# Performance work log

Measured on AMD Instinct MI355X. Metric: run time of the kernel, lower is better.

Reference implementation:

```python
import jax, jax.numpy as jnp
import numpy as np
from jax.scipy.special import logsumexp

B, T, N = 512, 1024, 64


def setup_inputs() -> dict:
    key = jax.random.key(0)
    k1, k2, k3, k4, k5, k6 = jax.random.split(key, 6)
    emit = jax.random.normal(k1, (B, T, N), dtype=jnp.float32)
    target = jax.random.randint(k2, (B, T), 0, N)
    # valid monotone mask: each sequence has length in [T//2, T], length >= 1
    lengths = jax.random.randint(k3, (B,), T // 2, T + 1)
    mask = jnp.arange(T)[None, :] < lengths[:, None]  # [B, T] bool
    trans = 0.1 * jax.random.normal(k4, (N, N), dtype=jnp.float32)
    strans = 0.1 * jax.random.normal(k5, (N,), dtype=jnp.float32)
    etrans = 0.1 * jax.random.normal(k6, (N,), dtype=jnp.float32)
    return {"emit": emit, "target": target, "mask": mask,
            "trans": trans, "strans": strans, "etrans": etrans}


def _get_logZ(emit_t, mask_t, trans, strans, etrans):
    # emit_t: [T, B, N], mask_t: [T, B]
    alpha0 = strans[None, :] + emit_t[0]  # [B, N]

    def step(alpha, inp):
        e_i, m_i = inp  # [B, N], [B]
        # scores[b, j] = logsumexp_i(alpha[b, i] + trans[i, j] + e_i[b, j])
        scores = logsumexp(alpha[:, :, None] + trans[None, :, :], axis=1) + e_i
        alpha = jnp.where(m_i[:, None], scores, alpha)
        return alpha, None

    alpha, _ = jax.lax.scan(step, alpha0, (emit_t[1:], mask_t[1:]))
    logZ = logsumexp(alpha + etrans[None, :], axis=1).sum()
    return logZ / B


def _get_score(emit_t, target_t, mask_t, trans, strans, etrans):
    # emit_t: [T, B, N], target_t/mask_t: [T, B]
    emit_scores = jnp.take_along_axis(emit_t, target_t[:, :, None], axis=2)[:, :, 0]  # [T, B]
    trans_scores = trans[target_t[:-1], target_t[1:]]  # [T-1, B]
    scores = emit_scores.at[1:].add(trans_scores)
    score = jnp.where(mask_t, scores, 0.0).sum()
    ends = mask_t.sum(axis=0) - 1  # [B]
    score = score + strans[target_t[0]].sum()
    last_tags = target_t[ends, jnp.arange(target_t.shape[1])]
    score = score + etrans[last_tags].sum()
    return score / B


def reference(emit, target, mask, trans, strans, etrans):
    # batch_first=True -> move to time-major [T, B, ...]
    emit_t = jnp.swapaxes(emit, 0, 1)
    target_t = target.T
    mask_t = mask.T
    logZ = _get_logZ(emit_t, mask_t, trans, strans, etrans)
    score = _get_score(emit_t, target_t, mask_t, trans, strans, etrans)
    return logZ - score
```

## Files before the change

kernel.cpp:

```cpp
#include <hip/hip_runtime.h>

#define Bn 512
#define Tn 1024
#define Nn 64
#define Kseg 8
#define BURN 16

typedef _Float16 h2 __attribute__((ext_vector_type(2)));
typedef _Float16 h8 __attribute__((ext_vector_type(8)));

#if __has_builtin(__builtin_amdgcn_fdot2)
__device__ __forceinline__ float fdot2f(h2 a, h2 b, float c) {
    return __builtin_amdgcn_fdot2(a, b, c, false);
}
#else
__device__ __forceinline__ float fdot2f(h2 a, h2 b, float c) {
    return fmaf((float)a[0], (float)b[0], fmaf((float)a[1], (float)b[1], c));
}
#endif

__device__ __forceinline__ float wave_sum(float v) {
#pragma unroll
    for (int off = 32; off >= 1; off >>= 1) v += __shfl_xor(v, off, 64);
    return v;
}

__global__ __launch_bounds__(64) void crf_seg(
    const float* __restrict__ emit,
    const int*   __restrict__ target,
    const int*   __restrict__ mask,
    const float* __restrict__ trans,
    const float* __restrict__ strans,
    const float* __restrict__ etrans,
    float*       __restrict__ out)
{
    __shared__ __align__(16) _Float16 pbuf[Nn];

    const int lane = threadIdx.x;
    const int b    = blockIdx.x & (Bn - 1);
    const int s    = blockIdx.x >> 9;

    h2 E2[32];
#pragma unroll
    for (int m = 0; m < 32; ++m) {
        float x0 = trans[(2 * m) * Nn + lane];
        float x1 = trans[(2 * m + 1) * Nn + lane];
        h2 e; e[0] = (_Float16)__expf(x0); e[1] = (_Float16)__expf(x1);
        E2[m] = e;
    }

    const int* mrow = mask + (size_t)b * Tn;
    int lsum = 0;
#pragma unroll
    for (int k = 0; k < Tn / Nn; ++k) lsum += mrow[k * Nn + lane];
#pragma unroll
    for (int off = 32; off >= 1; off >>= 1) lsum += __shfl_xor(lsum, off, 64);
    const int len = lsum;

    const int a_s = (s * len) >> 3;
    const int a_e = ((s + 1) * len) >> 3;
    const int tb   = s ? (a_s - BURN) : 1;
    const int tend = a_e - 1;
    const int rec_t = s ? a_s : -1;

    const size_t ebase = (size_t)b * Tn * Nn;

    float uu = s ? 1.0f : __expf(strans[lane]);
    int   S  = 0;
    float L0 = 0.0f;

    float wC[8], eN[8];
#pragma unroll
    for (int q = 0; q < 8; ++q) wC[q] = emit[ebase + (size_t)(tb - 1 + q) * Nn + lane];
#pragma unroll
    for (int q = 0; q < 8; ++q) eN[q] = emit[ebase + (size_t)(tb + 7 + q) * Nn + lane];
#pragma unroll
    for (int q = 0; q < 8; ++q) wC[q] = __expf(wC[q]);

    auto step = [&](float w) {
        int bits = __builtin_amdgcn_readfirstlane(__float_as_int(uu));
        int mk   = 127 - ((bits >> 23) & 0xff);
        S += mk;
        float p = ldexpf(uu, mk) * w;
        pbuf[lane] = (_Float16)p;

        const h8* pb8 = (const h8*)pbuf;
        float a0 = 0.f, a1 = 0.f, a2 = 0.f, a3 = 0.f;
        float a4 = 0.f, a5 = 0.f, a6 = 0.f, a7 = 0.f;
#pragma unroll
        for (int r = 0; r < 8; r += 2) {
            h8 v0 = pb8[r], v1 = pb8[r + 1];
            a0 = fdot2f(__builtin_shufflevector(v0, v0, 0, 1), E2[4 * r + 0], a0);
            a1 = fdot2f(__builtin_shufflevector(v0, v0, 2, 3), E2[4 * r + 1], a1);
            a2 = fdot2f(__builtin_shufflevector(v0, v0, 4, 5), E2[4 * r + 2], a2);
            a3 = fdot2f(__builtin_shufflevector(v0, v0, 6, 7), E2[4 * r + 3], a3);
            a4 = fdot2f(__builtin_shufflevector(v1, v1, 0, 1), E2[4 * r + 4], a4);
            a5 = fdot2f(__builtin_shufflevector(v1, v1, 2, 3), E2[4 * r + 5], a5);
            a6 = fdot2f(__builtin_shufflevector(v1, v1, 4, 5), E2[4 * r + 6], a6);
            a7 = fdot2f(__builtin_shufflevector(v1, v1, 6, 7), E2[4 * r + 7], a7);
        }
        uu = ((a0 + a1) + (a2 + a3)) + ((a4 + a5) + (a6 + a7));
    };

    int t0 = tb;
    while (t0 + 8 <= tend + 1) {
#pragma unroll
        for (int q = 0; q < 8; ++q) step(wC[q]);
#pragma unroll
        for (int q = 0; q < 8; ++q) wC[q] = __expf(eN[q]);
#pragma unroll
        for (int q = 0; q < 8; ++q) {
            int idx = t0 + 15 + q; if (idx > tend - 1) idx = tend - 1;
            eN[q] = emit[ebase + (size_t)idx * Nn + lane];
        }
        t0 += 8;
        if (t0 == rec_t) {
            L0 = __logf(wave_sum(uu));
            S = 0;
        }
    }
#pragma unroll
    for (int q = 0; q < 8; ++q)
        if (t0 + q <= tend) step(wC[q]);

    float lend;
    if (s == Kseg - 1) {
        float eL = emit[ebase + (size_t)(len - 1) * Nn + lane];
        lend = __logf(wave_sum(uu * __expf(eL + etrans[lane])));
    } else {
        lend = __logf(wave_sum(uu));
    }
    float contrib = lend - (float)S * 0.6931471805599453f - L0;

    const int* trow = target + (size_t)b * Tn;
    const int t_sc = s ? a_s : 0;
    float sc = 0.0f;
#pragma unroll
    for (int k = 0; k < 3; ++k) {
        int t = t_sc + k * Nn + lane;
        if (t < a_e) {
            int g = trow[t];
            sc += emit[ebase + (size_t)t * Nn + g];
            if (t > 0) sc += trans[trow[t - 1] * Nn + g];
        }
    }
    sc = wave_sum(sc);

    if (lane == 0) {
        if (s == 0)        sc += strans[trow[0]];
        if (s == Kseg - 1) sc += etrans[trow[len - 1]];
        atomicAdd(out, (contrib - sc) * (1.0f / (float)Bn));
    }
}

extern "C" void kernel_launch(void* const* d_in, const int* in_sizes, int n_in,
                              void* d_out, int out_size, void* d_ws, size_t ws_size,
                              hipStream_t stream) {
    const float* emit   = (const float*)d_in[0];
    const int*   target = (const int*)d_in[1];
    const int*   mask   = (const int*)d_in[2];
    const float* trans  = (const float*)d_in[3];
    const float* strans = (const float*)d_in[4];
    const float* etrans = (const float*)d_in[5];
    float* out = (float*)d_out;

    hipMemsetAsync(out, 0, sizeof(float), stream);
    crf_seg<<<Bn * Kseg, Nn, 0, stream>>>(emit, target, mask, trans, strans, etrans, out);
}
```

Measured before the change: 247.1 us.

## Batch 16 time segments per wave into MFMA matrix products

Replaces the 8-segment-per-sequence scheme, where each wave ran a matrix-vector recurrence with fdot2, with one wave per sequence. That wave advances 16 time segments at once as a 16-column matrix, multiplied by exp(trans) using 16x16x32 f16 MFMA instructions. Burn-in, rescaling by a shared power of two and per-segment log-sum recording are kept, and the end-transition weights are folded into the last segment. The goal is to swap scalar dot-product work for matrix-core throughput and cut the launched waves from 4096 to 512. In exchange, the shared max across columns may lose precision in f16 for columns far below the max. Each wave now also runs roughly len/16 plus burn-in steps with loads that are not prefetched.

```diff
diff --git a/kernel.cpp b/kernel.cpp
--- a/kernel.cpp
+++ b/kernel.cpp
@@ -3,21 +3,12 @@
 #define Bn 512
 #define Tn 1024
 #define Nn 64
-#define Kseg 8
 #define BURN 16
 
-typedef _Float16 h2 __attribute__((ext_vector_type(2)));
-typedef _Float16 h8 __attribute__((ext_vector_type(8)));
-
-#if __has_builtin(__builtin_amdgcn_fdot2)
-__device__ __forceinline__ float fdot2f(h2 a, h2 b, float c) {
-    return __builtin_amdgcn_fdot2(a, b, c, false);
-}
-#else
-__device__ __forceinline__ float fdot2f(h2 a, h2 b, float c) {
-    return fmaf((float)a[0], (float)b[0], fmaf((float)a[1], (float)b[1], c));
-}
-#endif
+typedef float    f4  __attribute__((ext_vector_type(4)));
+typedef __fp16   pk2 __attribute__((ext_vector_type(2)));
+typedef __fp16   pk4 __attribute__((ext_vector_type(4)));
+typedef _Float16 h8v __attribute__((ext_vector_type(8)));
 
 __device__ __forceinline__ float wave_sum(float v) {
 #pragma unroll
@@ -25,7 +16,7 @@
     return v;
 }
 
-__global__ __launch_bounds__(64) void crf_seg(
+__global__ __launch_bounds__(64) void crf_mfma(
     const float* __restrict__ emit,
     const int*   __restrict__ target,
     const int*   __restrict__ mask,
@@ -34,20 +25,25 @@
     const float* __restrict__ etrans,
     float*       __restrict__ out)
 {
-    __shared__ __align__(16) _Float16 pbuf[Nn];
+    __shared__ __align__(16) _Float16 plds[16 * 72];
 
     const int lane = threadIdx.x;
-    const int b    = blockIdx.x & (Bn - 1);
-    const int s    = blockIdx.x >> 9;
-
-    h2 E2[32];
-#pragma unroll
-    for (int m = 0; m < 32; ++m) {
-        float x0 = trans[(2 * m) * Nn + lane];
-        float x1 = trans[(2 * m + 1) * Nn + lane];
-        h2 e; e[0] = (_Float16)__expf(x0); e[1] = (_Float16)__expf(x1);
-        E2[m] = e;
-    }
+    const int n = lane & 15;
+    const int g = lane >> 4;
+    const int b = blockIdx.x;
+    const size_t ebase = (size_t)b * Tn * Nn;
+
+    h8v A[4][2];
+#pragma unroll
+    for (int r = 0; r < 4; ++r)
+#pragma unroll
+        for (int h = 0; h < 2; ++h) {
+            h8v a;
+#pragma unroll
+            for (int j = 0; j < 8; ++j)
+                a[j] = (_Float16)__expf(trans[(32 * h + 8 * g + j) * Nn + 16 * r + n]);
+            A[r][h] = a;
+        }
 
     const int* mrow = mask + (size_t)b * Tn;
     int lsum = 0;
@@ -57,99 +53,141 @@
     for (int off = 32; off >= 1; off >>= 1) lsum += __shfl_xor(lsum, off, 64);
     const int len = lsum;
 
-    const int a_s = (s * len) >> 3;
-    const int a_e = ((s + 1) * len) >> 3;
-    const int tb   = s ? (a_s - BURN) : 1;
-    const int tend = a_e - 1;
-    const int rec_t = s ? a_s : -1;
-
-    const size_t ebase = (size_t)b * Tn * Nn;
-
-    float uu = s ? 1.0f : __expf(strans[lane]);
-    int   S  = 0;
-    float L0 = 0.0f;
-
-    float wC[8], eN[8];
-#pragma unroll
-    for (int q = 0; q < 8; ++q) wC[q] = emit[ebase + (size_t)(tb - 1 + q) * Nn + lane];
-#pragma unroll
-    for (int q = 0; q < 8; ++q) eN[q] = emit[ebase + (size_t)(tb + 7 + q) * Nn + lane];
-#pragma unroll
-    for (int q = 0; q < 8; ++q) wC[q] = __expf(wC[q]);
-
-    auto step = [&](float w) {
-        int bits = __builtin_amdgcn_readfirstlane(__float_as_int(uu));
-        int mk   = 127 - ((bits >> 23) & 0xff);
+    const int a0    = (n * len) >> 4;
+    const int a1    = ((n + 1) * len) >> 4;
+    const int start = n ? (a0 - BURN) : 1;
+    const int tendv = a1 - 1;
+    const int maxk  = ((len + 15) >> 4) + BURN;
+
+    float wsel[4][4];
+#pragma unroll
+    for (int r = 0; r < 4; ++r) {
+        f4 ee = *(const f4*)(emit + ebase + (size_t)(len - 1) * Nn + 16 * r + 4 * g);
+        f4 et = *(const f4*)(etrans + 16 * r + 4 * g);
+#pragma unroll
+        for (int c = 0; c < 4; ++c)
+            wsel[r][c] = (n == 15) ? __expf(ee[c] + et[c]) : 1.0f;
+    }
+
+    float U[4][4];
+#pragma unroll
+    for (int r = 0; r < 4; ++r) {
+        f4 st = *(const f4*)(strans + 16 * r + 4 * g);
+#pragma unroll
+        for (int c = 0; c < 4; ++c)
+            U[r][c] = (n == 0) ? __expf(st[c]) : 1.0f;
+    }
+
+    int   S = 0;
+    float L0 = 0.0f, contrib = 0.0f;
+
+    f4 rb[4];
+    {
+        const int tr = start - 1;
+        const f4* p = (const f4*)(emit + ebase + (size_t)tr * Nn);
+#pragma unroll
+        for (int r = 0; r < 4; ++r) rb[r] = p[4 * r + g];
+    }
+    float Wx[4][4];
+#pragma unroll
+    for (int r = 0; r < 4; ++r)
+#pragma unroll
+        for (int c = 0; c < 4; ++c) Wx[r][c] = __expf(rb[r][c]);
+
+    const f4 zero4 = {0.f, 0.f, 0.f, 0.f};
+    _Float16* myCol = plds + n * 72;
+
+    for (int k = 0; k < maxk; ++k) {
+        {
+            int tr = start + k;
+            if (tr > Tn - 1) tr = Tn - 1;
+            const f4* p = (const f4*)(emit + ebase + (size_t)tr * Nn);
+#pragma unroll
+            for (int r = 0; r < 4; ++r) rb[r] = p[4 * r + g];
+        }
+
+        if (k == BURN) {
+            float cs = 0.f;
+#pragma unroll
+            for (int r = 0; r < 4; ++r)
+#pragma unroll
+                for (int c = 0; c < 4; ++c) cs += U[r][c];
+            cs += __shfl_xor(cs, 16, 64);
+            cs += __shfl_xor(cs, 32, 64);
+            float l0v = __logf(cs);
+            if (n) { L0 = l0v; S = 0; }
+        }
+
+        float mx = U[0][0];
+#pragma unroll
+        for (int r = 0; r < 4; ++r)
+#pragma unroll
+            for (int c = 0; c < 4; ++c) mx = fmaxf(mx, U[r][c]);
+        mx = fmaxf(mx, __shfl_xor(mx, 16, 64));
+        mx = fmaxf(mx, __shfl_xor(mx, 32, 64));
+        const int mk = 127 - ((__float_as_int(mx) >> 23) & 0xff);
         S += mk;
-        float p = ldexpf(uu, mk) * w;
-        pbuf[lane] = (_Float16)p;
-
-        const h8* pb8 = (const h8*)pbuf;
-        float a0 = 0.f, a1 = 0.f, a2 = 0.f, a3 = 0.f;
-        float a4 = 0.f, a5 = 0.f, a6 = 0.f, a7 = 0.f;
-#pragma unroll
-        for (int r = 0; r < 8; r += 2) {
-            h8 v0 = pb8[r], v1 = pb8[r + 1];
-            a0 = fdot2f(__builtin_shufflevector(v0, v0, 0, 1), E2[4 * r + 0], a0);
-            a1 = fdot2f(__builtin_shufflevector(v0, v0, 2, 3), E2[4 * r + 1], a1);
-            a2 = fdot2f(__builtin_shufflevector(v0, v0, 4, 5), E2[4 * r + 2], a2);
-            a3 = fdot2f(__builtin_shufflevector(v0, v0, 6, 7), E2[4 * r + 3], a3);
-            a4 = fdot2f(__builtin_shufflevector(v1, v1, 0, 1), E2[4 * r + 4], a4);
-            a5 = fdot2f(__builtin_shufflevector(v1, v1, 2, 3), E2[4 * r + 5], a5);
-            a6 = fdot2f(__builtin_shufflevector(v1, v1, 4, 5), E2[4 * r + 6], a6);
-            a7 = fdot2f(__builtin_shufflevector(v1, v1, 6, 7), E2[4 * r + 7], a7);
-        }
-        uu = ((a0 + a1) + (a2 + a3)) + ((a4 + a5) + (a6 + a7));
-    };
-
-    int t0 = tb;
-    while (t0 + 8 <= tend + 1) {
-#pragma unroll
-        for (int q = 0; q < 8; ++q) step(wC[q]);
-#pragma unroll
-        for (int q = 0; q < 8; ++q) wC[q] = __expf(eN[q]);
-#pragma unroll
-        for (int q = 0; q < 8; ++q) {
-            int idx = t0 + 15 + q; if (idx > tend - 1) idx = tend - 1;
-            eN[q] = emit[ebase + (size_t)idx * Nn + lane];
-        }
-        t0 += 8;
-        if (t0 == rec_t) {
-            L0 = __logf(wave_sum(uu));
-            S = 0;
-        }
-    }
-#pragma unroll
-    for (int q = 0; q < 8; ++q)
-        if (t0 + q <= tend) step(wC[q]);
-
-    float lend;
-    if (s == Kseg - 1) {
-        float eL = emit[ebase + (size_t)(len - 1) * Nn + lane];
-        lend = __logf(wave_sum(uu * __expf(eL + etrans[lane])));
-    } else {
-        lend = __logf(wave_sum(uu));
-    }
-    float contrib = lend - (float)S * 0.6931471805599453f - L0;
+
+#pragma unroll
+        for (int r = 0; r < 4; ++r) {
+            float p0 = U[r][0] * ldexpf(Wx[r][0], mk);
+            float p1 = U[r][1] * ldexpf(Wx[r][1], mk);
+            float p2 = U[r][2] * ldexpf(Wx[r][2], mk);
+            float p3 = U[r][3] * ldexpf(Wx[r][3], mk);
+            pk2 lo = __builtin_amdgcn_cvt_pkrtz(p0, p1);
+            pk2 hi = __builtin_amdgcn_cvt_pkrtz(p2, p3);
+            pk4 v4 = __builtin_shufflevector(lo, hi, 0, 1, 2, 3);
+            *(pk4*)&myCol[16 * r + 4 * g] = v4;
+        }
+
+        h8v B0 = *(const h8v*)&myCol[8 * g];
+        h8v B1 = *(const h8v*)&myCol[32 + 8 * g];
+
+#pragma unroll
+        for (int r = 0; r < 4; ++r) {
+            f4 acc = __builtin_amdgcn_mfma_f32_16x16x32_f16(A[r][0], B0, zero4, 0, 0, 0);
+            acc     = __builtin_amdgcn_mfma_f32_16x16x32_f16(A[r][1], B1, acc,   0, 0, 0);
+#pragma unroll
+            for (int c = 0; c < 4; ++c) U[r][c] = acc[c];
+        }
+
+        bool rec = (start + k) == tendv;
+        if (__any(rec)) {
+            float cs = 0.f;
+#pragma unroll
+            for (int r = 0; r < 4; ++r)
+#pragma unroll
+                for (int c = 0; c < 4; ++c) cs = fmaf(U[r][c], wsel[r][c], cs);
+            cs += __shfl_xor(cs, 16, 64);
+            cs += __shfl_xor(cs, 32, 64);
+            float lv = __logf(cs);
+            if (rec) contrib = lv - (float)S * 0.6931471805599453f - L0;
+        }
+
+#pragma unroll
+        for (int r = 0; r < 4; ++r)
+#pragma unroll
+            for (int c = 0; c < 4; ++c) Wx[r][c] = __expf(rb[r][c]);
+    }
+
+    float tot = wave_sum(contrib) * 0.25f;
 
     const int* trow = target + (size_t)b * Tn;
-    const int t_sc = s ? a_s : 0;
     float sc = 0.0f;
 #pragma unroll
-    for (int k = 0; k < 3; ++k) {
-        int t = t_sc + k * Nn + lane;
-        if (t < a_e) {
-            int g = trow[t];
-            sc += emit[ebase + (size_t)t * Nn + g];
-            if (t > 0) sc += trans[trow[t - 1] * Nn + g];
+    for (int k = 0; k < Tn / Nn; ++k) {
+        int t = k * Nn + lane;
+        if (t < len) {
+            int gT = trow[t];
+            sc += emit[ebase + (size_t)t * Nn + gT];
+            if (t > 0) sc += trans[trow[t - 1] * Nn + gT];
         }
     }
     sc = wave_sum(sc);
 
     if (lane == 0) {
-        if (s == 0)        sc += strans[trow[0]];
-        if (s == Kseg - 1) sc += etrans[trow[len - 1]];
-        atomicAdd(out, (contrib - sc) * (1.0f / (float)Bn));
+        sc += strans[trow[0]] + etrans[trow[len - 1]];
+        atomicAdd(out, (tot - sc) * (1.0f / (float)Bn));
     }
 }
 
@@ -164,6 +202,6 @@
     const float* etrans = (const float*)d_in[5];
     float* out = (float*)d_out;
 
-    hipMemsetAsync(out, 0, sizeof(float), stream);
-    crf_seg<<<Bn * Kseg, Nn, 0, stream>>>(emit, target, mask, trans, strans, etrans, out);
+    (void)hipMemsetAsync(out, 0, sizeof(float), stream);
+    crf_mfma<<<Bn, Nn, 0, stream>>>(emit, target, mask, trans, strans, etrans, out);
 }
```

New measurement: 241.6 us. 2.2% less time.
